# Performance work log

Measured on AMD Instinct MI355X. Metric: run time of the kernel, lower is better.

Reference implementation:

```python
import jax, jax.numpy as jnp
import numpy as np

EMBEDDING_DIM = 256
NUM_EMBEDDINGS = 8192
COMMITMENT_COST = 0.25
DECAY = 0.99
EPSILON = 1e-5


def setup_inputs() -> dict:
    key = jax.random.key(0)
    k1, k2 = jax.random.split(key)
    inputs = jax.random.normal(k1, (16, 32, 32, EMBEDDING_DIM), dtype=jnp.float32)
    # VarianceScaling(distribution='uniform'), fan_in scaling over [D, K]
    limit = float(np.sqrt(3.0 / EMBEDDING_DIM))
    embeddings = jax.random.uniform(k2, (EMBEDDING_DIM, NUM_EMBEDDINGS),
                                    minval=-limit, maxval=limit, dtype=jnp.float32)
    return {
        'inputs': inputs,
        'embeddings': embeddings,
        'ema_cs_hidden': jnp.zeros((NUM_EMBEDDINGS,), jnp.float32),
        'ema_dw_hidden': embeddings,  # hk initializes ema_dw to the embeddings
        'counter': 0,
        'is_training': 1,
    }


def reference(inputs, embeddings, ema_cs_hidden, ema_dw_hidden, counter, is_training):
    flat = inputs.reshape(-1, EMBEDDING_DIM)                        # [N, D]
    distances = (jnp.sum(flat ** 2, axis=1, keepdims=True)
                 - 2.0 * (flat @ embeddings)
                 + jnp.sum(embeddings ** 2, axis=0, keepdims=True))  # [N, K]
    encoding_indices = jnp.argmax(-distances, axis=1)                # [N]
    encodings = jax.nn.one_hot(encoding_indices, NUM_EMBEDDINGS,
                               dtype=distances.dtype)                # [N, K]
    idx = encoding_indices.reshape(inputs.shape[:-1])
    quantized = embeddings.T[idx]                                    # gather codebook
    e_latent_loss = jnp.mean((jax.lax.stop_gradient(quantized) - inputs) ** 2)
    loss = COMMITMENT_COST * e_latent_loss

    if is_training:
        # haiku ExponentialMovingAverage with zero-debias
        new_counter = counter + 1
        debias = 1.0 - DECAY ** new_counter
        cs_hidden = ema_cs_hidden * DECAY + jnp.sum(encodings, axis=0) * (1.0 - DECAY)
        cs_avg = cs_hidden / debias                                  # [K]
        dw = flat.T @ encodings                                      # [D, K] scatter-add as GEMM
        dw_hidden = ema_dw_hidden * DECAY + dw * (1.0 - DECAY)
        dw_avg = dw_hidden / debias
        n = jnp.sum(cs_avg)
        cs_norm = (cs_avg + EPSILON) / (n + NUM_EMBEDDINGS * EPSILON) * n
        new_embeddings = dw_avg / cs_norm[None, :]                   # [D, K]
    else:
        new_embeddings = embeddings

    # straight-through estimator
    quantized_st = inputs + jax.lax.stop_gradient(quantized - inputs)
    avg_probs = jnp.mean(encodings, axis=0)
    perplexity = jnp.exp(-jnp.sum(avg_probs * jnp.log(avg_probs + 1e-10)))
    return (quantized_st, loss, perplexity, idx, new_embeddings)
```

## Files before the change

kernel.cpp:

```cpp
#include <hip/hip_runtime.h>
#include <math.h>

#define DD 256
#define KK 8192
#define NN 16384
#define DECAYF 0.99f
#define EPSF 1e-5f
#define TAU 4e-3f

#define O_Q    0
#define O_LOSS 4194304
#define O_PERP 4194305
#define O_IDX  4194306
#define O_EMB  4210690

typedef float f32x4 __attribute__((ext_vector_type(4)));
typedef _Float16 f16x8 __attribute__((ext_vector_type(8)));

__device__ __forceinline__ unsigned short f2h(float f) {
  union { _Float16 h; unsigned short u; } c;
  c.h = (_Float16)f;
  return c.u;
}

__device__ __forceinline__ void gll16(const void* g, void* l) {
  __builtin_amdgcn_global_load_lds((const __attribute__((address_space(1))) void*)g,
                                   (__attribute__((address_space(3))) void*)l, 16, 0, 0);
}

__global__ void k_convert_x(const float* __restrict__ x, unsigned short* __restrict__ Ah,
                            float* __restrict__ esq, float* __restrict__ dwT,
                            float* __restrict__ counts, float* __restrict__ loss_part,
                            int* __restrict__ listc) {
  int tid = threadIdx.x;
  int i = blockIdx.x * 256 + tid;
  ((float2*)dwT)[i] = make_float2(0.f, 0.f);
  if (blockIdx.x < 32) esq[blockIdx.x * 256 + tid] = 0.f;
  else if (blockIdx.x < 64) counts[(blockIdx.x - 32) * 256 + tid] = 0.f;
  else if (blockIdx.x == 64) { loss_part[tid] = 0.f; if (tid == 0) *listc = 0; }
  float4 v = ((const float4*)x)[i];
  ushort4 h;
  h.x = f2h(v.x); h.y = f2h(v.y); h.z = f2h(v.z); h.w = f2h(v.w);
  ((ushort4*)Ah)[i] = h;
}

__global__ void k_convert_e(const float* __restrict__ emb, unsigned short* __restrict__ Eh,
                            float* __restrict__ embT, float* __restrict__ esq) {
  __shared__ float ld[32 * 33];
  int t = threadIdx.x;
  int k0 = blockIdx.x * 32, d0 = blockIdx.y * 32;
  {
    int din = t >> 3, kq = (t & 7) * 4;
    float4 v = *(const float4*)(emb + (size_t)(d0 + din) * KK + k0 + kq);
    ld[din * 33 + kq + 0] = v.x; ld[din * 33 + kq + 1] = v.y;
    ld[din * 33 + kq + 2] = v.z; ld[din * 33 + kq + 3] = v.w;
  }
  __syncthreads();
  int kout = t >> 3, dq = (t & 7) * 4;
  float f0 = ld[(dq + 0) * 33 + kout], f1 = ld[(dq + 1) * 33 + kout];
  float f2 = ld[(dq + 2) * 33 + kout], f3 = ld[(dq + 3) * 33 + kout];
  size_t o = (size_t)(k0 + kout) * DD + d0 + dq;
  float4 fv; fv.x = f0; fv.y = f1; fv.z = f2; fv.w = f3;
  *(float4*)(embT + o) = fv;
  ushort4 hv;
  hv.x = f2h(f0); hv.y = f2h(f1); hv.z = f2h(f2); hv.w = f2h(f3);
  *(ushort4*)(Eh + o) = hv;
  float p = (f0 * f0 + f1 * f1) + (f2 * f2 + f3 * f3);
  p += __shfl_xor(p, 1, 64);
  p += __shfl_xor(p, 2, 64);
  p += __shfl_xor(p, 4, 64);
  if ((t & 7) == 0) atomicAdd(esq + k0 + kout, p);
}

__launch_bounds__(256, 4)
__global__ void k_dist_mfma(const unsigned short* __restrict__ Ah, const unsigned short* __restrict__ Bh,
                            const float* __restrict__ esq,
                            float* __restrict__ part1, float* __restrict__ part2,
                            int* __restrict__ partidx) {
  __shared__ __align__(16) unsigned short sA[8192];
  __shared__ __align__(16) unsigned short sB[8192];

  const int tid = threadIdx.x;
  const int w = tid >> 6, lane = tid & 63;
  const int kb = blockIdx.x, nb = blockIdx.y;
  const int row0 = nb * 128, col0 = kb * 128;

  size_t gA[4], gB[4];
  int lbase[4];
  #pragma unroll
  for (int s = 0; s < 4; ++s) {
    int r = (w * 4 + s) * 8 + (lane >> 3);
    int c = (lane & 7) ^ (r & 7);
    gA[s] = (size_t)(row0 + r) * DD + c * 8;
    gB[s] = (size_t)(col0 + r) * DD + c * 8;
    lbase[s] = (w * 4 + s) * 512;
  }
  const int m = lane & 15, q = lane >> 4;

  f32x4 acc[2][8];
  #pragma unroll
  for (int i = 0; i < 2; ++i)
    #pragma unroll
    for (int j = 0; j < 8; ++j) acc[i][j] = (f32x4)0.f;

  for (int it = 0; it < 4; ++it) {
    const int d0 = it * 64;
    __syncthreads();
    #pragma unroll
    for (int s = 0; s < 4; ++s) {
      gll16(Ah + gA[s] + d0, sA + lbase[s]);
      gll16(Bh + gB[s] + d0, sB + lbase[s]);
    }
    __syncthreads();
    #pragma unroll
    for (int kk = 0; kk < 2; ++kk) {
      f16x8 a[2];
      #pragma unroll
      for (int i = 0; i < 2; ++i) {
        int wr = w * 32 + i * 16 + m;
        int slot = (kk * 4 + q) ^ (wr & 7);
        a[i] = *(const f16x8*)(sA + wr * 64 + slot * 8);
      }
      #pragma unroll
      for (int j = 0; j < 8; ++j) {
        int cn = j * 16 + m;
        int slot = (kk * 4 + q) ^ (cn & 7);
        f16x8 b = *(const f16x8*)(sB + cn * 64 + slot * 8);
        acc[0][j] = __builtin_amdgcn_mfma_f32_16x16x32_f16(a[0], b, acc[0][j], 0, 0, 0);
        acc[1][j] = __builtin_amdgcn_mfma_f32_16x16x32_f16(a[1], b, acc[1][j], 0, 0, 0);
      }
    }
  }

  float eq[8];
  #pragma unroll
  for (int j = 0; j < 8; ++j) eq[j] = esq[col0 + j * 16 + m];

  #pragma unroll
  for (int i = 0; i < 2; ++i) {
    #pragma unroll
    for (int reg = 0; reg < 4; ++reg) {
      float m1 = 3.402823466e+38f, m2 = 3.402823466e+38f;
      int bi = 0;
      #pragma unroll
      for (int j = 0; j < 8; ++j) {
        float dd = fmaf(-2.0f, acc[i][j][reg], eq[j]);
        if (dd < m1) { m2 = m1; m1 = dd; bi = col0 + j * 16 + m; }
        else if (dd < m2) m2 = dd;
      }
      #pragma unroll
      for (int st = 1; st < 16; st <<= 1) {
        float ov = __shfl_xor(m1, st, 64);
        int   oi = __shfl_xor(bi, st, 64);
        float o2 = __shfl_xor(m2, st, 64);
        float big = fmaxf(m1, ov);
        m2 = fminf(fminf(m2, o2), big);
        if (ov < m1 || (ov == m1 && oi < bi)) { m1 = ov; bi = oi; }
      }
      if (m == 0) {
        int prow = row0 + w * 32 + i * 16 + q * 4 + reg;
        int pidx = prow * 64 + kb;
        part1[pidx] = m1; part2[pidx] = m2; partidx[pidx] = bi;
      }
    }
  }
}

__global__ void k_argmin2(const float* __restrict__ part1, const float* __restrict__ part2,
                          const int* __restrict__ partidx, int* __restrict__ idxw,
                          int* __restrict__ listc, int* __restrict__ list,
                          unsigned long long* __restrict__ keys) {
  int w = threadIdx.x >> 6, l = threadIdx.x & 63;
  int row = blockIdx.x * 4 + w;
  int base = row * 64 + l;
  float m1 = part1[base], m2 = part2[base];
  int bi = partidx[base];
  #pragma unroll
  for (int st = 1; st < 64; st <<= 1) {
    float ov = __shfl_xor(m1, st, 64);
    int   oi = __shfl_xor(bi, st, 64);
    float o2 = __shfl_xor(m2, st, 64);
    float big = fmaxf(m1, ov);
    m2 = fminf(fminf(m2, o2), big);
    if (ov < m1 || (ov == m1 && oi < bi)) { m1 = ov; bi = oi; }
  }
  if (l == 0) {
    idxw[row] = bi;
    keys[row] = ~0ull;
    if (m2 - m1 < TAU) { int pos = atomicAdd(listc, 1); list[pos] = row; }
  }
}

__global__ void k_rescore(const float* __restrict__ x, const float* __restrict__ emb,
                          const int* __restrict__ listc, const int* __restrict__ list,
                          unsigned long long* __restrict__ keys) {
  __shared__ float se[8192];
  __shared__ double red[256];
  const int t = threadIdx.x;
  const int k0 = blockIdx.x * 32;
  #pragma unroll
  for (int i = 0; i < 32; ++i) {
    int elem = i * 256 + t;
    int d = elem >> 5, c = elem & 31;
    se[d * 32 + c] = emb[(size_t)d * KK + k0 + c];
  }
  __syncthreads();
  const int c = t & 31, p = t >> 5;
  int cnt = *listc;
  for (int li = blockIdx.y; li < cnt; li += gridDim.y) {
    int row = list[li];
    const float* xr = x + (size_t)row * DD;
    double acc = 0.0;
    #pragma unroll
    for (int j = 0; j < 32; ++j) {
      int d = p * 32 + j;
      double df = (double)xr[d] - (double)se[d * 32 + c];
      acc = fma(df, df, acc);
    }
    red[c * 8 + p] = acc;
    __syncthreads();
    if (t < 64) {
      unsigned long long key = ~0ull;
      if (t < 32) {
        double dist = 0.0;
        #pragma unroll
        for (int qq = 0; qq < 8; ++qq) dist += red[t * 8 + qq];
        key = ((unsigned long long)__double_as_longlong(dist) & ~0x1FFFull)
              | (unsigned long long)(k0 + t);
      }
      #pragma unroll
      for (int s = 1; s < 64; s <<= 1) {
        unsigned long long o = __shfl_xor(key, s, 64);
        if (o < key) key = o;
      }
      if (t == 0) atomicMin(&keys[row], key);
    }
    __syncthreads();
  }
}

__global__ void k_gather(const float* __restrict__ x, const float* __restrict__ embT,
                         const int* __restrict__ idxw, const unsigned long long* __restrict__ keys,
                         const int* __restrict__ train,
                         float* __restrict__ outq, float* __restrict__ outidx,
                         float* __restrict__ dwT, float* __restrict__ counts,
                         float* __restrict__ loss_part) {
  int w = threadIdx.x >> 6, l = threadIdx.x & 63;
  int n = blockIdx.x * 4 + w;
  unsigned long long kv = keys[n];
  int k = (kv != ~0ull) ? (int)(kv & 0x1FFFull) : idxw[n];
  float4 xv = ((const float4*)(x + (size_t)n * DD))[l];
  float4 qv = ((const float4*)(embT + (size_t)k * DD))[l];
  int d = l * 4;

  ((float4*)(outq + (size_t)n * DD))[l] = qv;

  float e0 = qv.x - xv.x, e1 = qv.y - xv.y, e2 = qv.z - xv.z, e3 = qv.w - xv.w;
  float ls = (e0 * e0 + e1 * e1) + (e2 * e2 + e3 * e3);

  if (*train) {
    const float wdw = 1.0f - DECAYF;
    float* base = dwT + (size_t)k * DD + d;
    atomicAdd(base + 0, xv.x * wdw);
    atomicAdd(base + 1, xv.y * wdw);
    atomicAdd(base + 2, xv.z * wdw);
    atomicAdd(base + 3, xv.w * wdw);
  }

  #pragma unroll
  for (int s = 1; s < 64; s <<= 1) ls += __shfl_xor(ls, s, 64);
  if (l == 0) {
    atomicAdd(&loss_part[blockIdx.x & 255], ls);
    atomicAdd(&counts[k], 1.0f);
    outidx[n] = (float)k;
  }
}

__global__ void k_stats(const float* __restrict__ counts, const float* __restrict__ ema_cs,
                        const int* __restrict__ counter, const int* __restrict__ train,
                        const float* __restrict__ loss_part, float* __restrict__ csn,
                        float* __restrict__ outloss, float* __restrict__ outperp) {
  __shared__ float s_n[4], s_e[4], s_l[4], s_tot[1];
  int tid = threadIdx.x;
  float debias = 1.0f - powf(DECAYF, (float)(*counter + 1));
  float nloc = 0.f, eloc = 0.f;
  float lloc = loss_part[tid];
  float avg[32];
  for (int i = 0; i < 32; ++i) {
    int k = tid + i * 256;
    float c = counts[k];
    float h = ema_cs[k] * DECAYF + c * (1.0f - DECAYF);
    float a = h / debias;
    avg[i] = a;
    nloc += a;
    float p = c * (1.0f / 16384.0f);
    eloc += p * logf(p + 1e-10f);
  }
  #pragma unroll
  for (int s = 1; s < 64; s <<= 1) {
    nloc += __shfl_xor(nloc, s, 64);
    eloc += __shfl_xor(eloc, s, 64);
    lloc += __shfl_xor(lloc, s, 64);
  }
  int w = tid >> 6, lane = tid & 63;
  if (lane == 0) { s_n[w] = nloc; s_e[w] = eloc; s_l[w] = lloc; }
  __syncthreads();
  if (tid == 0) {
    float nt = (s_n[0] + s_n[1]) + (s_n[2] + s_n[3]);
    float et = (s_e[0] + s_e[1]) + (s_e[2] + s_e[3]);
    float lt = (s_l[0] + s_l[1]) + (s_l[2] + s_l[3]);
    s_tot[0] = nt;
    outperp[0] = expf(-et);
    outloss[0] = 0.25f * (lt / 4194304.0f);
  }
  __syncthreads();
  float nsum = s_tot[0];
  float denom = nsum + 8192.0f * EPSF;
  for (int i = 0; i < 32; ++i) {
    int k = tid + i * 256;
    csn[k] = (avg[i] + EPSF) / denom * nsum;
  }
}

__global__ void k_final(const float* __restrict__ dwT, const float* __restrict__ ema_dw,
                        const float* __restrict__ emb, const float* __restrict__ csn,
                        const int* __restrict__ counter, const int* __restrict__ train,
                        float* __restrict__ out4) {
  __shared__ float ld[32 * 33];
  int t = threadIdx.x;
  int k0 = blockIdx.x * 32, d0 = blockIdx.y * 32;
  if (*train) {
    {
      int ki = t >> 3, dq = (t & 7) * 4;
      float4 v = *(const float4*)(dwT + (size_t)(k0 + ki) * DD + d0 + dq);
      ld[ki * 33 + dq + 0] = v.x; ld[ki * 33 + dq + 1] = v.y;
      ld[ki * 33 + dq + 2] = v.z; ld[ki * 33 + dq + 3] = v.w;
    }
    __syncthreads();
    int dout = t >> 3, kq = (t & 7) * 4;
    size_t o = (size_t)(d0 + dout) * KK + k0 + kq;
    float4 e = *(const float4*)(ema_dw + o);
    float4 c = *(const float4*)(csn + k0 + kq);
    float inv = 1.0f / (1.0f - powf(DECAYF, (float)(*counter + 1)));
    float4 r;
    r.x = fmaf(e.x, DECAYF, ld[(kq + 0) * 33 + dout]) * inv / c.x;
    r.y = fmaf(e.y, DECAYF, ld[(kq + 1) * 33 + dout]) * inv / c.y;
    r.z = fmaf(e.z, DECAYF, ld[(kq + 2) * 33 + dout]) * inv / c.z;
    r.w = fmaf(e.w, DECAYF, ld[(kq + 3) * 33 + dout]) * inv / c.w;
    *(float4*)(out4 + o) = r;
  } else {
    int dout = t >> 3, kq = (t & 7) * 4;
    size_t o = (size_t)(d0 + dout) * KK + k0 + kq;
    *(float4*)(out4 + o) = *(const float4*)(emb + o);
  }
}

extern "C" void kernel_launch(void* const* d_in, const int* in_sizes, int n_in,
                              void* d_out, int out_size, void* d_ws, size_t ws_size,
                              hipStream_t stream) {
  (void)in_sizes; (void)n_in; (void)out_size; (void)ws_size;
  const float* x      = (const float*)d_in[0];
  const float* emb    = (const float*)d_in[1];
  const float* ema_cs = (const float*)d_in[2];
  const float* ema_dw = (const float*)d_in[3];
  const int*   counter = (const int*)d_in[4];
  const int*   train   = (const int*)d_in[5];

  float* out = (float*)d_out;
  float* outq    = out + O_Q;
  float* outloss = out + O_LOSS;
  float* outperp = out + O_PERP;
  float* outidx  = out + O_IDX;
  float* out4    = out + O_EMB;

  char* W = (char*)d_ws;
  unsigned short* Ah   = (unsigned short*)(W);
  unsigned short* Eh   = (unsigned short*)(W + 8388608);
  float* embT          = (float*)(W + 12582912);
  float* part1         = (float*)(W + 20971520);
  float* part2         = (float*)(W + 25165824);
  int*   partidx       = (int*)(W + 29360128);
  float* dwT           = (float*)(W + 33554432);
  unsigned long long* keys = (unsigned long long*)(W + 41943040);
  float* esq           = (float*)(W + 42074112);
  float* csn           = (float*)(W + 42106880);
  float* counts        = (float*)(W + 42139648);
  float* loss_part     = (float*)(W + 42172416);
  int*   listc         = (int*)(W + 42173440);
  int*   list          = (int*)(W + 42173444);
  int*   idxw          = (int*)(W + 42238980);

  k_convert_x<<<4096, 256, 0, stream>>>(x, Ah, esq, dwT, counts, loss_part, listc);
  k_convert_e<<<dim3(256, 8), 256, 0, stream>>>(emb, Eh, embT, esq);
  k_dist_mfma<<<dim3(64, 128), 256, 0, stream>>>(Ah, Eh, esq, part1, part2, partidx);
  k_argmin2<<<4096, 256, 0, stream>>>(part1, part2, partidx, idxw, listc, list, keys);
  k_rescore<<<dim3(256, 8), 256, 0, stream>>>(x, emb, listc, list, keys);
  k_gather<<<4096, 256, 0, stream>>>(x, embT, idxw, keys, train, outq, outidx, dwT, counts, loss_part);
  k_stats<<<1, 256, 0, stream>>>(counts, ema_cs, counter, train, loss_part, csn, outloss, outperp);
  k_final<<<dim3(256, 8), 256, 0, stream>>>(dwT, ema_dw, emb, csn, counter, train, out4);
}
```

Baseline: 397.6 us.

## Replace atomic dw scatter with counting-sort segmented sum; enlarge distance GEMM tile

The per-element float atomicAdd scatter into dwT is replaced by a bucket sort. One kernel computes indices and counts, another takes a prefix sum to get per-code offsets, the gather kernel appends row ids into per-code lists, and one block per code sums its assigned rows without atomics. Separately, the distance GEMM tile grows from 128x128 to 256x128 rows per block with launch bounds lowered to 2, so each B tile is reused across more rows. The change adds two kernel launches and a serial single-block prefix pass. Per-code summation is sequential, so a few heavily used codes could become stragglers.

After: 394.5 us. No clear change (-0.8%).

```diff
diff --git a/kernel.cpp b/kernel.cpp
--- a/kernel.cpp
+++ b/kernel.cpp
@@ -29,12 +29,10 @@
 }
 
 __global__ void k_convert_x(const float* __restrict__ x, unsigned short* __restrict__ Ah,
-                            float* __restrict__ esq, float* __restrict__ dwT,
-                            float* __restrict__ counts, float* __restrict__ loss_part,
-                            int* __restrict__ listc) {
+                            float* __restrict__ esq, float* __restrict__ counts,
+                            float* __restrict__ loss_part, int* __restrict__ listc) {
   int tid = threadIdx.x;
   int i = blockIdx.x * 256 + tid;
-  ((float2*)dwT)[i] = make_float2(0.f, 0.f);
   if (blockIdx.x < 32) esq[blockIdx.x * 256 + tid] = 0.f;
   else if (blockIdx.x < 64) counts[(blockIdx.x - 32) * 256 + tid] = 0.f;
   else if (blockIdx.x == 64) { loss_part[tid] = 0.f; if (tid == 0) *listc = 0; }
@@ -72,34 +70,40 @@
   if ((t & 7) == 0) atomicAdd(esq + k0 + kout, p);
 }
 
-__launch_bounds__(256, 4)
+__launch_bounds__(256, 2)
 __global__ void k_dist_mfma(const unsigned short* __restrict__ Ah, const unsigned short* __restrict__ Bh,
                             const float* __restrict__ esq,
                             float* __restrict__ part1, float* __restrict__ part2,
                             int* __restrict__ partidx) {
-  __shared__ __align__(16) unsigned short sA[8192];
-  __shared__ __align__(16) unsigned short sB[8192];
+  __shared__ __align__(16) unsigned short sA[256 * 64];
+  __shared__ __align__(16) unsigned short sB[128 * 64];
 
   const int tid = threadIdx.x;
   const int w = tid >> 6, lane = tid & 63;
   const int kb = blockIdx.x, nb = blockIdx.y;
-  const int row0 = nb * 128, col0 = kb * 128;
-
-  size_t gA[4], gB[4];
-  int lbase[4];
-  #pragma unroll
-  for (int s = 0; s < 4; ++s) {
-    int r = (w * 4 + s) * 8 + (lane >> 3);
+  const int row0 = nb * 256, col0 = kb * 128;
+
+  size_t gA[8]; int lA[8];
+  #pragma unroll
+  for (int s = 0; s < 8; ++s) {
+    int r = s * 32 + w * 8 + (lane >> 3);
     int c = (lane & 7) ^ (r & 7);
     gA[s] = (size_t)(row0 + r) * DD + c * 8;
+    lA[s] = r * 64 + (lane & 7) * 8;
+  }
+  size_t gB[4]; int lB[4];
+  #pragma unroll
+  for (int s = 0; s < 4; ++s) {
+    int r = s * 32 + w * 8 + (lane >> 3);
+    int c = (lane & 7) ^ (r & 7);
     gB[s] = (size_t)(col0 + r) * DD + c * 8;
-    lbase[s] = (w * 4 + s) * 512;
+    lB[s] = r * 64 + (lane & 7) * 8;
   }
   const int m = lane & 15, q = lane >> 4;
 
-  f32x4 acc[2][8];
-  #pragma unroll
-  for (int i = 0; i < 2; ++i)
+  f32x4 acc[4][8];
+  #pragma unroll
+  for (int i = 0; i < 4; ++i)
     #pragma unroll
     for (int j = 0; j < 8; ++j) acc[i][j] = (f32x4)0.f;
 
@@ -107,27 +111,26 @@
     const int d0 = it * 64;
     __syncthreads();
     #pragma unroll
-    for (int s = 0; s < 4; ++s) {
-      gll16(Ah + gA[s] + d0, sA + lbase[s]);
-      gll16(Bh + gB[s] + d0, sB + lbase[s]);
-    }
+    for (int s = 0; s < 8; ++s) gll16(Ah + gA[s] + d0, sA + lA[s]);
+    #pragma unroll
+    for (int s = 0; s < 4; ++s) gll16(Bh + gB[s] + d0, sB + lB[s]);
     __syncthreads();
     #pragma unroll
     for (int kk = 0; kk < 2; ++kk) {
-      f16x8 a[2];
+      const int kc = kk * 4 + q;
+      f16x8 a[4];
       #pragma unroll
-      for (int i = 0; i < 2; ++i) {
-        int wr = w * 32 + i * 16 + m;
-        int slot = (kk * 4 + q) ^ (wr & 7);
-        a[i] = *(const f16x8*)(sA + wr * 64 + slot * 8);
+      for (int i = 0; i < 4; ++i) {
+        int wr = w * 64 + i * 16 + m;
+        a[i] = *(const f16x8*)(sA + wr * 64 + (kc ^ (wr & 7)) * 8);
       }
       #pragma unroll
       for (int j = 0; j < 8; ++j) {
         int cn = j * 16 + m;
-        int slot = (kk * 4 + q) ^ (cn & 7);
-        f16x8 b = *(const f16x8*)(sB + cn * 64 + slot * 8);
-        acc[0][j] = __builtin_amdgcn_mfma_f32_16x16x32_f16(a[0], b, acc[0][j], 0, 0, 0);
-        acc[1][j] = __builtin_amdgcn_mfma_f32_16x16x32_f16(a[1], b, acc[1][j], 0, 0, 0);
+        f16x8 b = *(const f16x8*)(sB + cn * 64 + (kc ^ (cn & 7)) * 8);
+        #pragma unroll
+        for (int i = 0; i < 4; ++i)
+          acc[i][j] = __builtin_amdgcn_mfma_f32_16x16x32_f16(a[i], b, acc[i][j], 0, 0, 0);
       }
     }
   }
@@ -137,7 +140,7 @@
   for (int j = 0; j < 8; ++j) eq[j] = esq[col0 + j * 16 + m];
 
   #pragma unroll
-  for (int i = 0; i < 2; ++i) {
+  for (int i = 0; i < 4; ++i) {
     #pragma unroll
     for (int reg = 0; reg < 4; ++reg) {
       float m1 = 3.402823466e+38f, m2 = 3.402823466e+38f;
@@ -158,7 +161,7 @@
         if (ov < m1 || (ov == m1 && oi < bi)) { m1 = ov; bi = oi; }
       }
       if (m == 0) {
-        int prow = row0 + w * 32 + i * 16 + q * 4 + reg;
+        int prow = row0 + w * 64 + i * 16 + q * 4 + reg;
         int pidx = prow * 64 + kb;
         part1[pidx] = m1; part2[pidx] = m2; partidx[pidx] = bi;
       }
@@ -239,95 +242,128 @@
   }
 }
 
+__global__ void k_index(int* __restrict__ idxw, const unsigned long long* __restrict__ keys,
+                        float* __restrict__ counts) {
+  int n = blockIdx.x * 256 + threadIdx.x;
+  unsigned long long kv = keys[n];
+  int k = (kv != ~0ull) ? (int)(kv & 0x1FFFull) : idxw[n];
+  idxw[n] = k;
+  atomicAdd(&counts[k], 1.0f);
+}
+
+__global__ void k_prefix(const float* __restrict__ counts, const float* __restrict__ ema_cs,
+                         const int* __restrict__ counter,
+                         float* __restrict__ csn, float* __restrict__ outperp,
+                         int* __restrict__ base, int* __restrict__ cursor) {
+  __shared__ int s_sum[4], s_woff[4];
+  __shared__ float s_n[4], s_e[4], s_nsum;
+  int t = threadIdx.x, w = t >> 6, lane = t & 63;
+  float debias = 1.0f - powf(DECAYF, (float)(*counter + 1));
+  int pre[32]; int run = 0; float nloc = 0.f, eloc = 0.f;
+  for (int i = 0; i < 32; ++i) {
+    int k = t * 32 + i;
+    float c = counts[k];
+    run += (int)c; pre[i] = run;
+    nloc += (ema_cs[k] * DECAYF + c * (1.0f - DECAYF)) / debias;
+    float p = c * (1.0f / 16384.0f);
+    eloc += p * logf(p + 1e-10f);
+  }
+  int inc = run;
+  #pragma unroll
+  for (int d = 1; d < 64; d <<= 1) {
+    int v = __shfl(inc, lane - d, 64);
+    if (lane >= d) inc += v;
+  }
+  int excl = inc - run;
+  int wtot = __shfl(inc, 63, 64);
+  float ns = nloc, es = eloc;
+  #pragma unroll
+  for (int d = 1; d < 64; d <<= 1) { ns += __shfl_xor(ns, d, 64); es += __shfl_xor(es, d, 64); }
+  if (lane == 0) { s_sum[w] = wtot; s_n[w] = ns; s_e[w] = es; }
+  __syncthreads();
+  if (t == 0) {
+    int off = 0;
+    #pragma unroll
+    for (int ww = 0; ww < 4; ++ww) { s_woff[ww] = off; off += s_sum[ww]; }
+    float nt = (s_n[0] + s_n[1]) + (s_n[2] + s_n[3]);
+    float et = (s_e[0] + s_e[1]) + (s_e[2] + s_e[3]);
+    s_nsum = nt;
+    outperp[0] = expf(-et);
+  }
+  __syncthreads();
+  int tbase = s_woff[w] + excl;
+  float nsum = s_nsum;
+  float denom = nsum + 8192.0f * EPSF;
+  for (int i = 0; i < 32; ++i) {
+    int k = t * 32 + i;
+    float c = counts[k];
+    int b = tbase + pre[i] - (int)c;
+    base[k] = b; cursor[k] = b;
+    float a = (ema_cs[k] * DECAYF + c * (1.0f - DECAYF)) / debias;
+    csn[k] = (a + EPSF) / denom * nsum;
+  }
+}
+
 __global__ void k_gather(const float* __restrict__ x, const float* __restrict__ embT,
-                         const int* __restrict__ idxw, const unsigned long long* __restrict__ keys,
-                         const int* __restrict__ train,
+                         const int* __restrict__ idxw, const int* __restrict__ train,
                          float* __restrict__ outq, float* __restrict__ outidx,
-                         float* __restrict__ dwT, float* __restrict__ counts,
+                         int* __restrict__ rowlist, int* __restrict__ cursor,
                          float* __restrict__ loss_part) {
   int w = threadIdx.x >> 6, l = threadIdx.x & 63;
   int n = blockIdx.x * 4 + w;
-  unsigned long long kv = keys[n];
-  int k = (kv != ~0ull) ? (int)(kv & 0x1FFFull) : idxw[n];
+  int k = idxw[n];
   float4 xv = ((const float4*)(x + (size_t)n * DD))[l];
   float4 qv = ((const float4*)(embT + (size_t)k * DD))[l];
-  int d = l * 4;
 
   ((float4*)(outq + (size_t)n * DD))[l] = qv;
 
   float e0 = qv.x - xv.x, e1 = qv.y - xv.y, e2 = qv.z - xv.z, e3 = qv.w - xv.w;
   float ls = (e0 * e0 + e1 * e1) + (e2 * e2 + e3 * e3);
-
-  if (*train) {
-    const float wdw = 1.0f - DECAYF;
-    float* base = dwT + (size_t)k * DD + d;
-    atomicAdd(base + 0, xv.x * wdw);
-    atomicAdd(base + 1, xv.y * wdw);
-    atomicAdd(base + 2, xv.z * wdw);
-    atomicAdd(base + 3, xv.w * wdw);
-  }
-
   #pragma unroll
   for (int s = 1; s < 64; s <<= 1) ls += __shfl_xor(ls, s, 64);
   if (l == 0) {
     atomicAdd(&loss_part[blockIdx.x & 255], ls);
-    atomicAdd(&counts[k], 1.0f);
     outidx[n] = (float)k;
-  }
-}
-
-__global__ void k_stats(const float* __restrict__ counts, const float* __restrict__ ema_cs,
-                        const int* __restrict__ counter, const int* __restrict__ train,
-                        const float* __restrict__ loss_part, float* __restrict__ csn,
-                        float* __restrict__ outloss, float* __restrict__ outperp) {
-  __shared__ float s_n[4], s_e[4], s_l[4], s_tot[1];
-  int tid = threadIdx.x;
-  float debias = 1.0f - powf(DECAYF, (float)(*counter + 1));
-  float nloc = 0.f, eloc = 0.f;
-  float lloc = loss_part[tid];
-  float avg[32];
-  for (int i = 0; i < 32; ++i) {
-    int k = tid + i * 256;
-    float c = counts[k];
-    float h = ema_cs[k] * DECAYF + c * (1.0f - DECAYF);
-    float a = h / debias;
-    avg[i] = a;
-    nloc += a;
-    float p = c * (1.0f / 16384.0f);
-    eloc += p * logf(p + 1e-10f);
-  }
-  #pragma unroll
-  for (int s = 1; s < 64; s <<= 1) {
-    nloc += __shfl_xor(nloc, s, 64);
-    eloc += __shfl_xor(eloc, s, 64);
-    lloc += __shfl_xor(lloc, s, 64);
-  }
-  int w = tid >> 6, lane = tid & 63;
-  if (lane == 0) { s_n[w] = nloc; s_e[w] = eloc; s_l[w] = lloc; }
-  __syncthreads();
-  if (tid == 0) {
-    float nt = (s_n[0] + s_n[1]) + (s_n[2] + s_n[3]);
-    float et = (s_e[0] + s_e[1]) + (s_e[2] + s_e[3]);
-    float lt = (s_l[0] + s_l[1]) + (s_l[2] + s_l[3]);
-    s_tot[0] = nt;
-    outperp[0] = expf(-et);
-    outloss[0] = 0.25f * (lt / 4194304.0f);
-  }
-  __syncthreads();
-  float nsum = s_tot[0];
-  float denom = nsum + 8192.0f * EPSF;
-  for (int i = 0; i < 32; ++i) {
-    int k = tid + i * 256;
-    csn[k] = (avg[i] + EPSF) / denom * nsum;
-  }
+    if (*train) {
+      int pos = atomicAdd(&cursor[k], 1);
+      rowlist[pos] = n;
+    }
+  }
+}
+
+__global__ void k_dw(const float* __restrict__ x, const int* __restrict__ base,
+                     const float* __restrict__ counts, const int* __restrict__ rowlist,
+                     const int* __restrict__ train, float* __restrict__ dwT) {
+  if (!*train) return;
+  int c = blockIdx.x, l = threadIdx.x;
+  int b0 = base[c], cnt = (int)counts[c];
+  float4 acc = make_float4(0.f, 0.f, 0.f, 0.f);
+  for (int i = 0; i < cnt; ++i) {
+    int row = rowlist[b0 + i];
+    float4 v = ((const float4*)(x + (size_t)row * DD))[l];
+    acc.x += v.x; acc.y += v.y; acc.z += v.z; acc.w += v.w;
+  }
+  const float wdw = 1.0f - DECAYF;
+  acc.x *= wdw; acc.y *= wdw; acc.z *= wdw; acc.w *= wdw;
+  ((float4*)(dwT + (size_t)c * DD))[l] = acc;
 }
 
 __global__ void k_final(const float* __restrict__ dwT, const float* __restrict__ ema_dw,
                         const float* __restrict__ emb, const float* __restrict__ csn,
                         const int* __restrict__ counter, const int* __restrict__ train,
+                        const float* __restrict__ loss_part, float* __restrict__ outloss,
                         float* __restrict__ out4) {
   __shared__ float ld[32 * 33];
+  __shared__ float sl[4];
   int t = threadIdx.x;
+  if (blockIdx.x == 0 && blockIdx.y == 0) {
+    float ll = loss_part[t];
+    #pragma unroll
+    for (int d = 1; d < 64; d <<= 1) ll += __shfl_xor(ll, d, 64);
+    if ((t & 63) == 0) sl[t >> 6] = ll;
+    __syncthreads();
+    if (t == 0) outloss[0] = 0.25f * (((sl[0] + sl[1]) + (sl[2] + sl[3])) / 4194304.0f);
+  }
   int k0 = blockIdx.x * 32, d0 = blockIdx.y * 32;
   if (*train) {
     {
@@ -389,13 +425,18 @@
   int*   listc         = (int*)(W + 42173440);
   int*   list          = (int*)(W + 42173444);
   int*   idxw          = (int*)(W + 42238980);
-
-  k_convert_x<<<4096, 256, 0, stream>>>(x, Ah, esq, dwT, counts, loss_part, listc);
+  int*   rowlist       = (int*)(W + 42304516);
+  int*   basea         = (int*)(W + 42370052);
+  int*   cursor        = (int*)(W + 42402820);
+
+  k_convert_x<<<4096, 256, 0, stream>>>(x, Ah, esq, counts, loss_part, listc);
   k_convert_e<<<dim3(256, 8), 256, 0, stream>>>(emb, Eh, embT, esq);
-  k_dist_mfma<<<dim3(64, 128), 256, 0, stream>>>(Ah, Eh, esq, part1, part2, partidx);
+  k_dist_mfma<<<dim3(64, 64), 256, 0, stream>>>(Ah, Eh, esq, part1, part2, partidx);
   k_argmin2<<<4096, 256, 0, stream>>>(part1, part2, partidx, idxw, listc, list, keys);
   k_rescore<<<dim3(256, 8), 256, 0, stream>>>(x, emb, listc, list, keys);
-  k_gather<<<4096, 256, 0, stream>>>(x, embT, idxw, keys, train, outq, outidx, dwT, counts, loss_part);
-  k_stats<<<1, 256, 0, stream>>>(counts, ema_cs, counter, train, loss_part, csn, outloss, outperp);
-  k_final<<<dim3(256, 8), 256, 0, stream>>>(dwT, ema_dw, emb, csn, counter, train, out4);
-}
+  k_index<<<64, 256, 0, stream>>>(idxw, keys, counts);
+  k_prefix<<<1, 256, 0, stream>>>(counts, ema_cs, counter, csn, outperp, basea, cursor);
+  k_gather<<<4096, 256, 0, stream>>>(x, embT, idxw, train, outq, outidx, rowlist, cursor, loss_part);
+  k_dw<<<8192, 64, 0, stream>>>(x, basea, counts, rowlist, train, dwT);
+  k_final<<<dim3(256, 8), 256, 0, stream>>>(dwT, ema_dw, emb, csn, counter, train, loss_part, outloss, out4);
+}
```
